# Performance work log

Hardware: AMD Instinct MI355X
Metric: run time of the kernel (lower is better)

Reference implementation:

```python
import jax, jax.numpy as jnp
import numpy as np

B, S, H = 2, 2048, 2048
NH, NKV, HD = 32, 8, 64
G = NH // NKV  # query heads per KV head
SCALE = HD ** -0.5
NEG = -1e9


def setup_inputs() -> dict:
    key = jax.random.key(0)
    ks = jax.random.split(key, 6)
    hidden_states = jax.random.normal(ks[0], (B, S, H), dtype=jnp.float32)
    # causal additive mask, broadcastable over batch and heads
    causal = jnp.tril(jnp.ones((S, S), dtype=bool))
    attention_mask = jnp.where(causal, 0.0, NEG).astype(jnp.float32)[None, None]
    sd = 1.0 / np.sqrt(H)
    wq = jax.random.normal(ks[1], (H, NH * HD), dtype=jnp.float32) * sd
    wk = jax.random.normal(ks[2], (H, NKV * HD), dtype=jnp.float32) * sd
    wv = jax.random.normal(ks[3], (H, NKV * HD), dtype=jnp.float32) * sd
    wo = jax.random.normal(ks[4], (NH * HD, H), dtype=jnp.float32) * sd
    return {"hidden_states": hidden_states, "attention_mask": attention_mask,
            "wq": wq, "wk": wk, "wv": wv, "wo": wo}


def reference(hidden_states, attention_mask, wq, wk, wv, wo):
    b, s, _ = hidden_states.shape
    # projections; group q heads as [b, kv_head, group, s, d] to avoid
    # materializing expanded K/V (same math as expand+matmul)
    q = (hidden_states @ wq).reshape(b, s, NKV, G, HD)
    k = (hidden_states @ wk).reshape(b, s, NKV, HD)
    v = (hidden_states @ wv).reshape(b, s, NKV, HD)
    q = jnp.einsum('bskgd->bkgsd', q)
    k = jnp.einsum('bskd->bksd', k)
    v = jnp.einsum('bskd->bksd', v)
    scores = jnp.einsum('bkgsd,bktd->bkgst', q, k) * SCALE  # [b,kv,G,s,s]
    mask = attention_mask  # [1,1,S,S] broadcastable
    scores = scores + mask[:, :, None] if mask.ndim == 4 else scores + mask
    attn = jax.nn.softmax(scores.astype(jnp.float32), axis=-1).astype(q.dtype)
    out = jnp.einsum('bkgst,bktd->bkgsd', attn, v)
    out = jnp.einsum('bkgsd->bskgd', out).reshape(b, s, NH * HD)
    return out @ wo
```

## Files before the change

### kernel.cpp

```cpp
#include <hip/hip_runtime.h>
#include <hip/hip_bf16.h>
#include <type_traits>


#define B_SZ 2
#define S_LEN 2048
#define HID 2048
#define NHEADS 32
#define NKVH 8
#define HEADD 64
#define QKV_N 3072
#define QK_SCALE 0.18033688f
#define FIXED_M 12.0f

typedef __attribute__((ext_vector_type(8))) short bf16x8;
typedef __attribute__((ext_vector_type(4))) float f32x4;

__device__ __forceinline__ float bf2f(unsigned short u) {
  union { unsigned int i; float f; } v;
  v.i = ((unsigned int)u) << 16;
  return v.f;
}
__device__ __forceinline__ unsigned short f2bf(float f) {
  union { float f; unsigned int i; } v;
  v.f = f;
  unsigned int r = v.i + 0x7fffu + ((v.i >> 16) & 1u);
  return (unsigned short)(r >> 16);
}
#if __has_builtin(__builtin_amdgcn_exp2f)
__device__ __forceinline__ float exp2v(float x) { return __builtin_amdgcn_exp2f(x); }
#else
__device__ __forceinline__ float exp2v(float x) { return exp2f(x); }
#endif
__device__ __forceinline__ void gload_lds16(const unsigned short* g, unsigned short* l) {
  __builtin_amdgcn_global_load_lds(
      (const __attribute__((address_space(1))) unsigned int*)g,
      (__attribute__((address_space(3))) unsigned int*)l, 16, 0, 0);
}
__device__ __forceinline__ int pv_perm(int s) {
  return (((s >> 2) & 7) << 3) | (((s >> 5) & 1) << 2) | (s & 3);
}

__global__ void cvt_bf16_kernel(const float4* __restrict__ in,
                                ushort4* __restrict__ out, int n4) {
  int i = blockIdx.x * blockDim.x + threadIdx.x;
  if (i >= n4) return;
  float4 v = in[i];
  ushort4 o;
  o.x = f2bf(v.x); o.y = f2bf(v.y); o.z = f2bf(v.z); o.w = f2bf(v.w);
  out[i] = o;
}

__global__ void transpose_qkvw_kernel(const float* __restrict__ wq,
                                      const float* __restrict__ wk,
                                      const float* __restrict__ wv,
                                      unsigned short* __restrict__ out) {
  __shared__ float tile[32][33];
  int n0 = blockIdx.x * 32;
  int r0 = blockIdx.y * 32;
  const float* src;
  int C, cb;
  float scale;
  if (n0 < 2048) { src = wq; C = 2048; cb = n0; scale = QK_SCALE; }
  else if (n0 < 2560) { src = wk; C = 512; cb = n0 - 2048; scale = 1.0f; }
  else { src = wv; C = 512; cb = n0 - 2560; scale = 1.0f; }
  int x = threadIdx.x, y = threadIdx.y;
#pragma unroll
  for (int i = 0; i < 32; i += 8)
    tile[y + i][x] = src[(size_t)(r0 + y + i) * C + cb + x];
  __syncthreads();
#pragma unroll
  for (int i = 0; i < 32; i += 8)
    out[(size_t)(n0 + y + i) * HID + r0 + x] = f2bf(tile[x][y + i] * scale);
}

__global__ void transpose_cvt_kernel(const float* __restrict__ in,
                                     unsigned short* __restrict__ out,
                                     int R, int C) {
  __shared__ float tile[32][33];
  int c0 = blockIdx.x * 32, r0 = blockIdx.y * 32;
  int x = threadIdx.x, y = threadIdx.y;
#pragma unroll
  for (int i = 0; i < 32; i += 8)
    tile[y + i][x] = in[(size_t)(r0 + y + i) * C + c0 + x];
  __syncthreads();
#pragma unroll
  for (int i = 0; i < 32; i += 8)
    out[(size_t)(c0 + y + i) * R + r0 + x] = f2bf(tile[x][y + i]);
}

__global__ void transpose_v_kernel(const unsigned short* __restrict__ QKV,
                                   unsigned short* __restrict__ Vt) {
  __shared__ unsigned short tile[32][33];
  int s0 = blockIdx.x * 32, d0 = blockIdx.y * 32;
  int bk = blockIdx.z;
  int b = bk >> 3, kvh = bk & 7;
  int x = threadIdx.x, y = threadIdx.y;
#pragma unroll
  for (int i = 0; i < 32; i += 8)
    tile[y + i][x] =
        QKV[(size_t)(b * S_LEN + s0 + y + i) * QKV_N + 2560 + kvh * HEADD + d0 + x];
  __syncthreads();
  int colg = s0 + x;
  int colp = (colg & ~63) | pv_perm(colg & 63);
#pragma unroll
  for (int i = 0; i < 32; i += 8)
    Vt[((size_t)(b * NKVH + kvh) * HEADD + d0 + y + i) * S_LEN + colp] =
        tile[x][y + i];
}

template <typename OutT>
__global__ __launch_bounds__(256) void gemm_bt_kernel(
    const unsigned short* __restrict__ A, const unsigned short* __restrict__ Bt,
    OutT* __restrict__ C, int M, int N, int K) {
  __shared__ unsigned short ldsA[3][128 * 32];
  __shared__ unsigned short ldsB[3][128 * 32];
  const int tid = threadIdx.x;
  const int wave = tid >> 6;
  const int lane = tid & 63;
  const int nwg = gridDim.x;
  const int orig = blockIdx.x;
  const int swz = (orig & 7) * (nwg >> 3) + (orig >> 3);
  const int ntn = N >> 7;
  const int m0 = (swz / ntn) << 7;
  const int n0 = (swz % ntn) << 7;
  const int wr = wave >> 1, wc = wave & 1;
  f32x4 acc[4][4] = {};

  size_t offA[2], offB[2];
#pragma unroll
  for (int i = 0; i < 2; ++i) {
    int cc = tid + i * 256;
    int row = cc >> 2, slot = cc & 3;
    int xk = (slot ^ ((row >> 1) & 3)) * 8;
    offA[i] = (size_t)(m0 + row) * K + xk;
    offB[i] = (size_t)(n0 + row) * K + xk;
  }
  const int rl = lane & 15, g = lane >> 4;
  const int nk = K >> 5;
  const int ldsbase = (wave * 64) * 8;

#pragma unroll
  for (int s = 0; s < 2; ++s) {
#pragma unroll
    for (int i = 0; i < 2; ++i) {
      gload_lds16(A + offA[i] + (s << 5), &ldsA[s][ldsbase + i * 256 * 8]);
      gload_lds16(Bt + offB[i] + (s << 5), &ldsB[s][ldsbase + i * 256 * 8]);
    }
  }
  int cur = 0;

  for (int t = 0; t < nk; ++t) {
    __builtin_amdgcn_sched_barrier(0);
    if (t < nk - 1)
      asm volatile("s_waitcnt vmcnt(4)" ::: "memory");
    else
      asm volatile("s_waitcnt vmcnt(0)" ::: "memory");
    __builtin_amdgcn_s_barrier();
    __builtin_amdgcn_sched_barrier(0);
    if (t + 2 < nk) {
      const int k0 = (t + 2) << 5;
      const int nb = (cur + 2 >= 3) ? cur - 1 : cur + 2;
#pragma unroll
      for (int i = 0; i < 2; ++i) {
        gload_lds16(A + offA[i] + k0, &ldsA[nb][ldsbase + i * 256 * 8]);
        gload_lds16(Bt + offB[i] + k0, &ldsB[nb][ldsbase + i * 256 * 8]);
      }
    }
    const int xs = (g ^ ((rl >> 1) & 3)) * 8;
    bf16x8 a[4], b[4];
#pragma unroll
    for (int mi = 0; mi < 4; ++mi)
      a[mi] = *(const bf16x8*)&ldsA[cur][(wr * 64 + mi * 16 + rl) * 32 + xs];
#pragma unroll
    for (int ni = 0; ni < 4; ++ni)
      b[ni] = *(const bf16x8*)&ldsB[cur][(wc * 64 + ni * 16 + rl) * 32 + xs];
#pragma unroll
    for (int mi = 0; mi < 4; ++mi)
#pragma unroll
      for (int ni = 0; ni < 4; ++ni)
        acc[mi][ni] =
            __builtin_amdgcn_mfma_f32_16x16x32_bf16(a[mi], b[ni], acc[mi][ni], 0, 0, 0);
    cur = (cur + 1 == 3) ? 0 : cur + 1;
  }
#pragma unroll
  for (int mi = 0; mi < 4; ++mi)
#pragma unroll
    for (int ni = 0; ni < 4; ++ni)
#pragma unroll
      for (int r = 0; r < 4; ++r) {
        int row = m0 + wr * 64 + mi * 16 + (lane >> 4) * 4 + r;
        int col = n0 + wc * 64 + ni * 16 + (lane & 15);
        float v = acc[mi][ni][r];
        if constexpr (std::is_same_v<OutT, unsigned short>)
          C[(size_t)row * N + col] = f2bf(v);
        else
          C[(size_t)row * N + col] = v;
      }
}

__global__ __launch_bounds__(256) void mfma_attn_kernel(
    const unsigned short* __restrict__ QKV,
    const unsigned short* __restrict__ Vt,
    unsigned short* __restrict__ O) {
  __shared__ unsigned short Ks[2][64 * 64];
  __shared__ unsigned short Vs[2][64 * 64];
  const int head = blockIdx.y, b = blockIdx.z;
  const int kvh = head >> 2;
  const int tid = threadIdx.x;
  const int w = tid >> 6, lane = tid & 63;
  const int c = lane & 15, g = lane >> 4;
  const int srow = tid >> 3, sslot = tid & 7;
  const int xslot = sslot ^ (srow & 7);

  const unsigned short* Ksrc[2];
  const unsigned short* Vsrc[2];
#pragma unroll
  for (int i = 0; i < 2; ++i) {
    int row = srow + i * 32;
    Ksrc[i] = QKV + (size_t)(b * S_LEN + row) * QKV_N + 2048 + kvh * HEADD + xslot * 8;
    Vsrc[i] = Vt + ((size_t)(b * NKVH + kvh) * HEADD + row) * S_LEN + xslot * 8;
  }

#pragma unroll
  for (int i = 0; i < 2; ++i) {
    gload_lds16(Ksrc[i], &Ks[0][(w * 64 + i * 256) * 8]);
    gload_lds16(Vsrc[i], &Vs[0][(w * 64 + i * 256) * 8]);
  }
  __syncthreads();
  int cur = 0;

  for (int ph = 0; ph < 2; ++ph) {
    const int qt = (ph == 0) ? (int)blockIdx.x : (S_LEN / 64 - 1) - (int)blockIdx.x;
    bf16x8 qf[2];
    {
      const unsigned short* qp =
          QKV + (size_t)(b * S_LEN + qt * 64 + w * 16 + c) * QKV_N + head * HEADD +
          g * 8;
      qf[0] = *(const bf16x8*)(qp);
      qf[1] = *(const bf16x8*)(qp + 32);
    }
    f32x4 o_acc[4] = {};
    float lpart = 0.f;

    for (int t = 0; t <= qt; ++t) {
      const int kv0 = t * 64;
      const bool has_next = !(ph == 1 && t == qt);
      if (has_next) {
        const int kvn = (t < qt) ? kv0 + 64 : 0;
        const int nb = cur ^ 1;
#pragma unroll
        for (int i = 0; i < 2; ++i) {
          gload_lds16(Ksrc[i] + (size_t)kvn * QKV_N, &Ks[nb][(w * 64 + i * 256) * 8]);
          gload_lds16(Vsrc[i] + kvn, &Vs[nb][(w * 64 + i * 256) * 8]);
        }
      }
      f32x4 s_acc[4] = {};
      __builtin_amdgcn_s_setprio(1);
#pragma unroll
      for (int ks = 0; ks < 2; ++ks)
#pragma unroll
        for (int kn = 0; kn < 4; ++kn) {
          bf16x8 kf = *(const bf16x8*)&Ks[cur][(kn * 16 + c) * 64 +
                                              (((ks * 4 + g) ^ (c & 7)) * 8)];
          s_acc[kn] =
              __builtin_amdgcn_mfma_f32_16x16x32_bf16(kf, qf[ks], s_acc[kn], 0, 0, 0);
        }
      __builtin_amdgcn_s_setprio(0);
      if (t == qt) {
        const int qg = qt * 64 + w * 16 + c;
#pragma unroll
        for (int kn = 0; kn < 4; ++kn)
#pragma unroll
          for (int r = 0; r < 4; ++r)
            if (kv0 + kn * 16 + g * 4 + r > qg) s_acc[kn][r] = -1e30f;
      }
      float p[4][4];
#pragma unroll
      for (int kn = 0; kn < 4; ++kn)
#pragma unroll
        for (int r = 0; r < 4; ++r) {
          p[kn][r] = exp2v(s_acc[kn][r] - FIXED_M);
          lpart += p[kn][r];
        }
      union { bf16x8 v; unsigned int w4[4]; } afu[2];
#pragma unroll
      for (int b2 = 0; b2 < 2; ++b2) {
        afu[b2].w4[0] = __builtin_amdgcn_perm(__float_as_uint(p[b2][1]),
                                              __float_as_uint(p[b2][0]), 0x07060302u);
        afu[b2].w4[1] = __builtin_amdgcn_perm(__float_as_uint(p[b2][3]),
                                              __float_as_uint(p[b2][2]), 0x07060302u);
        afu[b2].w4[2] = __builtin_amdgcn_perm(__float_as_uint(p[2 + b2][1]),
                                              __float_as_uint(p[2 + b2][0]), 0x07060302u);
        afu[b2].w4[3] = __builtin_amdgcn_perm(__float_as_uint(p[2 + b2][3]),
                                              __float_as_uint(p[2 + b2][2]), 0x07060302u);
      }
      __builtin_amdgcn_s_setprio(1);
#pragma unroll
      for (int ks2 = 0; ks2 < 2; ++ks2)
#pragma unroll
        for (int dn = 0; dn < 4; ++dn) {
          bf16x8 vf = *(const bf16x8*)&Vs[cur][(dn * 16 + c) * 64 +
                                              (((ks2 * 4 + g) ^ (c & 7)) * 8)];
          o_acc[dn] =
              __builtin_amdgcn_mfma_f32_16x16x32_bf16(afu[ks2].v, vf, o_acc[dn], 0, 0, 0);
        }
      __builtin_amdgcn_s_setprio(0);
      __syncthreads();
      if (has_next) cur ^= 1;
    }
    float lsum = lpart;
    lsum += __shfl_xor(lsum, 16);
    lsum += __shfl_xor(lsum, 32);
    float inv = 1.0f / lsum;
    float invr[4];
#pragma unroll
    for (int r = 0; r < 4; ++r) invr[r] = __shfl(inv, g * 4 + r);
#pragma unroll
    for (int dn = 0; dn < 4; ++dn)
#pragma unroll
      for (int r = 0; r < 4; ++r) {
        int row = qt * 64 + w * 16 + g * 4 + r;
        int col = head * HEADD + dn * 16 + c;
        O[(size_t)(b * S_LEN + row) * (NHEADS * HEADD) + col] =
            f2bf(o_acc[dn][r] * invr[r]);
      }
  }
}

extern "C" void kernel_launch(void* const* d_in, const int* in_sizes, int n_in,
                              void* d_out, int out_size, void* d_ws, size_t ws_size,
                              hipStream_t stream) {
  const float* hs = (const float*)d_in[0];
  const float* wq = (const float*)d_in[2];
  const float* wk = (const float*)d_in[3];
  const float* wv = (const float*)d_in[4];
  const float* wo = (const float*)d_in[5];
  float* out = (float*)d_out;

  char* ws = (char*)d_ws;
  unsigned short* hs_bf = (unsigned short*)(ws);
  unsigned short* wAllT = (unsigned short*)(ws + ((size_t)16 << 20));
  unsigned short* woT  = (unsigned short*)(ws + ((size_t)28 << 20));
  unsigned short* QKV  = (unsigned short*)(ws + ((size_t)36 << 20));
  unsigned short* Ab   = (unsigned short*)(ws + ((size_t)60 << 20));
  unsigned short* VtB  = (unsigned short*)(ws + ((size_t)76 << 20));

  int n4 = (B_SZ * S_LEN * HID) / 4;
  cvt_bf16_kernel<<<n4 / 256, 256, 0, stream>>>((const float4*)hs, (ushort4*)hs_bf, n4);

  dim3 tb(32, 8);
  transpose_qkvw_kernel<<<dim3(96, 64), tb, 0, stream>>>(wq, wk, wv, wAllT);
  transpose_cvt_kernel<<<dim3(64, 64), tb, 0, stream>>>(wo, woT, NHEADS * HEADD, HID);

  gemm_bt_kernel<unsigned short><<<32 * 24, 256, 0, stream>>>(
      hs_bf, wAllT, QKV, B_SZ * S_LEN, QKV_N, HID);

  transpose_v_kernel<<<dim3(S_LEN / 32, HEADD / 32, B_SZ * NKVH), tb, 0, stream>>>(
      QKV, VtB);

  mfma_attn_kernel<<<dim3(S_LEN / 128, NHEADS, B_SZ), 256, 0, stream>>>(QKV, VtB, Ab);

  gemm_bt_kernel<float><<<32 * 16, 256, 0, stream>>>(
      Ab, woT, out, B_SZ * S_LEN, HID, HID);
}
```

Measured before the change: 197.7 us.

## Replace 128x128 GEMM with 256x256-tile 8-wave kernel using interleaved prefetch

Swaps the 128x128-tile, 4-wave GEMM for a 256x256-tile, 8-wave kernel with a K step of 64, double-buffered in 128 KB of dynamic LDS. Global-to-LDS loads are spread between the MFMA groups, and s_setprio is raised around the MFMA blocks. The larger tiles give more reuse per byte loaded and fewer barriers per FLOP. In exchange, the QKV GEMM launches only 192 workgroups and the output GEMM only 128, fewer than the number of CUs, so part of the GPU sits idle and there is more register pressure per thread.

After: 195.7 us. About the same (-1.0%).

```diff
diff --git a/kernel.cpp b/kernel.cpp
--- a/kernel.cpp
+++ b/kernel.cpp
@@ -110,88 +110,158 @@
 }
 
 template <typename OutT>
-__global__ __launch_bounds__(256) void gemm_bt_kernel(
+__global__ __launch_bounds__(512, 2) void gemm256_kernel(
     const unsigned short* __restrict__ A, const unsigned short* __restrict__ Bt,
-    OutT* __restrict__ C, int M, int N, int K) {
-  __shared__ unsigned short ldsA[3][128 * 32];
-  __shared__ unsigned short ldsB[3][128 * 32];
+    OutT* __restrict__ C, int N, int K) {
+  extern __shared__ unsigned short sm[];
   const int tid = threadIdx.x;
   const int wave = tid >> 6;
   const int lane = tid & 63;
+  const int wm = wave >> 2, wn = wave & 3;
+  const int rl = lane & 15, g = lane >> 4;
   const int nwg = gridDim.x;
   const int orig = blockIdx.x;
   const int swz = (orig & 7) * (nwg >> 3) + (orig >> 3);
-  const int ntn = N >> 7;
-  const int m0 = (swz / ntn) << 7;
-  const int n0 = (swz % ntn) << 7;
-  const int wr = wave >> 1, wc = wave & 1;
-  f32x4 acc[4][4] = {};
-
-  size_t offA[2], offB[2];
+  const int ntn = N >> 8;
+  const int m0 = (swz / ntn) << 8;
+  const int n0 = (swz % ntn) << 8;
+  f32x4 acc[8][4] = {};
+
+  size_t aoff[2], boff[2];
+  int ldst[2];
 #pragma unroll
   for (int i = 0; i < 2; ++i) {
-    int cc = tid + i * 256;
+    int cc = tid + i * 512;
     int row = cc >> 2, slot = cc & 3;
     int xk = (slot ^ ((row >> 1) & 3)) * 8;
-    offA[i] = (size_t)(m0 + row) * K + xk;
-    offB[i] = (size_t)(n0 + row) * K + xk;
+    aoff[i] = (size_t)(m0 + row) * K + xk;
+    boff[i] = (size_t)(n0 + row) * K + xk;
+    ldst[i] = (wave * 64 + i * 512) * 8;
   }
-  const int rl = lane & 15, g = lane >> 4;
-  const int nk = K >> 5;
-  const int ldsbase = (wave * 64) * 8;
-
-#pragma unroll
-  for (int s = 0; s < 2; ++s) {
-#pragma unroll
-    for (int i = 0; i < 2; ++i) {
-      gload_lds16(A + offA[i] + (s << 5), &ldsA[s][ldsbase + i * 256 * 8]);
-      gload_lds16(Bt + offB[i] + (s << 5), &ldsB[s][ldsbase + i * 256 * 8]);
-    }
-  }
+  const int NT = K >> 6;
+
+#pragma unroll
+  for (int i = 0; i < 2; ++i) gload_lds16(A + aoff[i], sm + ldst[i]);
+#pragma unroll
+  for (int i = 0; i < 2; ++i) gload_lds16(Bt + boff[i], sm + 32768 + ldst[i]);
+#pragma unroll
+  for (int i = 0; i < 2; ++i) gload_lds16(A + aoff[i] + 32, sm + 8192 + ldst[i]);
+#pragma unroll
+  for (int i = 0; i < 2; ++i) gload_lds16(Bt + boff[i] + 32, sm + 40960 + ldst[i]);
+
   int cur = 0;
-
-  for (int t = 0; t < nk; ++t) {
+  for (int t = 0; t < NT; ++t) {
+    const int nxt = cur ^ 1;
+    const bool st = (t + 1 < NT);
+    const size_t k1 = (size_t)(t + 1) << 6;
+    unsigned short* An0 = sm + (nxt * 2 + 0) * 8192;
+    unsigned short* An1 = sm + (nxt * 2 + 1) * 8192;
+    unsigned short* Bn0 = sm + 32768 + (nxt * 2 + 0) * 8192;
+    unsigned short* Bn1 = sm + 32768 + (nxt * 2 + 1) * 8192;
+    const unsigned short* Ac0 = sm + (cur * 2 + 0) * 8192;
+    const unsigned short* Ac1 = sm + (cur * 2 + 1) * 8192;
+    const unsigned short* Bc0 = sm + 32768 + (cur * 2 + 0) * 8192;
+    const unsigned short* Bc1 = sm + 32768 + (cur * 2 + 1) * 8192;
+    bf16x8 bA[4], bB[4];
+    if (st) {
+      gload_lds16(A + aoff[0] + k1, An0 + ldst[0]);
+      gload_lds16(A + aoff[1] + k1, An0 + ldst[1]);
+    }
     __builtin_amdgcn_sched_barrier(0);
-    if (t < nk - 1)
-      asm volatile("s_waitcnt vmcnt(4)" ::: "memory");
-    else
-      asm volatile("s_waitcnt vmcnt(0)" ::: "memory");
+    if (st) asm volatile("s_waitcnt vmcnt(6)" ::: "memory");
+    else    asm volatile("s_waitcnt vmcnt(4)" ::: "memory");
     __builtin_amdgcn_s_barrier();
     __builtin_amdgcn_sched_barrier(0);
-    if (t + 2 < nk) {
-      const int k0 = (t + 2) << 5;
-      const int nb = (cur + 2 >= 3) ? cur - 1 : cur + 2;
-#pragma unroll
-      for (int i = 0; i < 2; ++i) {
-        gload_lds16(A + offA[i] + k0, &ldsA[nb][ldsbase + i * 256 * 8]);
-        gload_lds16(Bt + offB[i] + k0, &ldsB[nb][ldsbase + i * 256 * 8]);
-      }
-    }
-    const int xs = (g ^ ((rl >> 1) & 3)) * 8;
-    bf16x8 a[4], b[4];
+#pragma unroll
+    for (int nb = 0; nb < 4; ++nb) {
+      int rw = wn * 64 + nb * 16 + rl;
+      bB[nb] = *(const bf16x8*)&Bc0[rw * 32 + (g ^ ((rw >> 1) & 3)) * 8];
+    }
+#pragma unroll
+    for (int mi = 0; mi < 4; ++mi) {
+      int rw = wm * 128 + mi * 16 + rl;
+      bA[mi] = *(const bf16x8*)&Ac0[rw * 32 + (g ^ ((rw >> 1) & 3)) * 8];
+    }
+    __builtin_amdgcn_s_setprio(1);
 #pragma unroll
     for (int mi = 0; mi < 4; ++mi)
-      a[mi] = *(const bf16x8*)&ldsA[cur][(wr * 64 + mi * 16 + rl) * 32 + xs];
-#pragma unroll
-    for (int ni = 0; ni < 4; ++ni)
-      b[ni] = *(const bf16x8*)&ldsB[cur][(wc * 64 + ni * 16 + rl) * 32 + xs];
+#pragma unroll
+      for (int nb = 0; nb < 4; ++nb)
+        acc[mi][nb] = __builtin_amdgcn_mfma_f32_16x16x32_bf16(bA[mi], bB[nb],
+                                                              acc[mi][nb], 0, 0, 0);
+    __builtin_amdgcn_s_setprio(0);
+    if (st) {
+      gload_lds16(Bt + boff[0] + k1, Bn0 + ldst[0]);
+      gload_lds16(Bt + boff[1] + k1, Bn0 + ldst[1]);
+    }
+#pragma unroll
+    for (int mi = 0; mi < 4; ++mi) {
+      int rw = wm * 128 + 64 + mi * 16 + rl;
+      bA[mi] = *(const bf16x8*)&Ac0[rw * 32 + (g ^ ((rw >> 1) & 3)) * 8];
+    }
+    __builtin_amdgcn_s_setprio(1);
 #pragma unroll
     for (int mi = 0; mi < 4; ++mi)
 #pragma unroll
-      for (int ni = 0; ni < 4; ++ni)
-        acc[mi][ni] =
-            __builtin_amdgcn_mfma_f32_16x16x32_bf16(a[mi], b[ni], acc[mi][ni], 0, 0, 0);
-    cur = (cur + 1 == 3) ? 0 : cur + 1;
+      for (int nb = 0; nb < 4; ++nb)
+        acc[4 + mi][nb] = __builtin_amdgcn_mfma_f32_16x16x32_bf16(bA[mi], bB[nb],
+                                                                  acc[4 + mi][nb], 0, 0, 0);
+    __builtin_amdgcn_s_setprio(0);
+    if (st) {
+      gload_lds16(A + aoff[0] + k1 + 32, An1 + ldst[0]);
+      gload_lds16(A + aoff[1] + k1 + 32, An1 + ldst[1]);
+    }
+    __builtin_amdgcn_sched_barrier(0);
+    if (st) asm volatile("s_waitcnt vmcnt(6)" ::: "memory");
+    else    asm volatile("s_waitcnt vmcnt(0)" ::: "memory");
+    __builtin_amdgcn_s_barrier();
+    __builtin_amdgcn_sched_barrier(0);
+#pragma unroll
+    for (int nb = 0; nb < 4; ++nb) {
+      int rw = wn * 64 + nb * 16 + rl;
+      bB[nb] = *(const bf16x8*)&Bc1[rw * 32 + (g ^ ((rw >> 1) & 3)) * 8];
+    }
+#pragma unroll
+    for (int mi = 0; mi < 4; ++mi) {
+      int rw = wm * 128 + mi * 16 + rl;
+      bA[mi] = *(const bf16x8*)&Ac1[rw * 32 + (g ^ ((rw >> 1) & 3)) * 8];
+    }
+    __builtin_amdgcn_s_setprio(1);
+#pragma unroll
+    for (int mi = 0; mi < 4; ++mi)
+#pragma unroll
+      for (int nb = 0; nb < 4; ++nb)
+        acc[mi][nb] = __builtin_amdgcn_mfma_f32_16x16x32_bf16(bA[mi], bB[nb],
+                                                              acc[mi][nb], 0, 0, 0);
+    __builtin_amdgcn_s_setprio(0);
+    if (st) {
+      gload_lds16(Bt + boff[0] + k1 + 32, Bn1 + ldst[0]);
+      gload_lds16(Bt + boff[1] + k1 + 32, Bn1 + ldst[1]);
+    }
+#pragma unroll
+    for (int mi = 0; mi < 4; ++mi) {
+      int rw = wm * 128 + 64 + mi * 16 + rl;
+      bA[mi] = *(const bf16x8*)&Ac1[rw * 32 + (g ^ ((rw >> 1) & 3)) * 8];
+    }
+    __builtin_amdgcn_s_setprio(1);
+#pragma unroll
+    for (int mi = 0; mi < 4; ++mi)
+#pragma unroll
+      for (int nb = 0; nb < 4; ++nb)
+        acc[4 + mi][nb] = __builtin_amdgcn_mfma_f32_16x16x32_bf16(bA[mi], bB[nb],
+                                                                  acc[4 + mi][nb], 0, 0, 0);
+    __builtin_amdgcn_s_setprio(0);
+    cur = nxt;
   }
 #pragma unroll
-  for (int mi = 0; mi < 4; ++mi)
-#pragma unroll
-    for (int ni = 0; ni < 4; ++ni)
+  for (int mg = 0; mg < 8; ++mg)
+#pragma unroll
+    for (int nb = 0; nb < 4; ++nb)
 #pragma unroll
       for (int r = 0; r < 4; ++r) {
-        int row = m0 + wr * 64 + mi * 16 + (lane >> 4) * 4 + r;
-        int col = n0 + wc * 64 + ni * 16 + (lane & 15);
-        float v = acc[mi][ni][r];
+        int row = m0 + wm * 128 + (mg >> 2) * 64 + (mg & 3) * 16 + g * 4 + r;
+        int col = n0 + wn * 64 + nb * 16 + rl;
+        float v = acc[mg][nb][r];
         if constexpr (std::is_same_v<OutT, unsigned short>)
           C[(size_t)row * N + col] = f2bf(v);
         else
@@ -338,6 +408,11 @@
   const float* wo = (const float*)d_in[5];
   float* out = (float*)d_out;
 
+  hipFuncSetAttribute(reinterpret_cast<const void*>(gemm256_kernel<unsigned short>),
+                      hipFuncAttributeMaxDynamicSharedMemorySize, 131072);
+  hipFuncSetAttribute(reinterpret_cast<const void*>(gemm256_kernel<float>),
+                      hipFuncAttributeMaxDynamicSharedMemorySize, 131072);
+
   char* ws = (char*)d_ws;
   unsigned short* hs_bf = (unsigned short*)(ws);
   unsigned short* wAllT = (unsigned short*)(ws + ((size_t)16 << 20));
@@ -353,14 +428,14 @@
   transpose_qkvw_kernel<<<dim3(96, 64), tb, 0, stream>>>(wq, wk, wv, wAllT);
   transpose_cvt_kernel<<<dim3(64, 64), tb, 0, stream>>>(wo, woT, NHEADS * HEADD, HID);
 
-  gemm_bt_kernel<unsigned short><<<32 * 24, 256, 0, stream>>>(
-      hs_bf, wAllT, QKV, B_SZ * S_LEN, QKV_N, HID);
+  gemm256_kernel<unsigned short><<<192, 512, 131072, stream>>>(
+      hs_bf, wAllT, QKV, QKV_N, HID);
 
   transpose_v_kernel<<<dim3(S_LEN / 32, HEADD / 32, B_SZ * NKVH), tb, 0, stream>>>(
       QKV, VtB);
 
   mfma_attn_kernel<<<dim3(S_LEN / 128, NHEADS, B_SZ), 256, 0, stream>>>(QKV, VtB, Ab);
 
-  gemm_bt_kernel<float><<<32 * 16, 256, 0, stream>>>(
-      Ab, woT, out, B_SZ * S_LEN, HID, HID);
-}
+  gemm256_kernel<float><<<128, 512, 131072, stream>>>(
+      Ab, woT, out, HID, HID);
+}
```
